# Kernel optimization log

Measured on AMD Instinct MI355X. Metric: run time of the kernel, lower is better.

The kernel has to match this reference:

```python
import jax, jax.numpy as jnp
import numpy as np

B, SEQ, P, D, H, DH, HID = 65536, 2, 1009, 256, 4, 64, 1024
ATT_RATE = 0.5

def setup_inputs() -> dict:
    key = jax.random.key(0)
    ks = jax.random.split(key, 18)
    init_range = 0.02
    lin = lambda k, shape, fan_in: jax.random.uniform(k, shape, jnp.float32, -1.0, 1.0) / np.sqrt(fan_in)
    return {
        "x": jax.random.randint(ks[0], (B, SEQ), 0, P),
        "tok_emb": jax.random.normal(ks[1], (P, D), jnp.float32) / np.sqrt(D),
        "pos_emb": jax.random.normal(ks[2], (SEQ, D), jnp.float32) / np.sqrt(D),
        "W_Q": init_range * jax.random.normal(ks[3], (H, D, DH), jnp.float32),
        "W_K": init_range * jax.random.normal(ks[4], (H, D, DH), jnp.float32),
        "W_V": init_range * jax.random.normal(ks[5], (H, D, DH), jnp.float32),
        "W_O": init_range * jax.random.normal(ks[6], (H, DH, D), jnp.float32),
        "b_Q": jnp.zeros((H, DH), jnp.float32),
        "b_K": jnp.zeros((H, DH), jnp.float32),
        "b_V": jnp.zeros((H, DH), jnp.float32),
        "b_O": jnp.zeros((D,), jnp.float32),
        "fc1_w": lin(ks[7], (HID, D), D),
        "fc1_b": lin(ks[8], (HID,), D),
        "fc2_w": lin(ks[9], (D, HID), HID),
        "fc2_b": lin(ks[10], (D,), HID),
        "un_w": lin(ks[11], (P, D), D),
        "un_b": lin(ks[12], (P,), D),
    }

def reference(x, tok_emb, pos_emb, W_Q, W_K, W_V, W_O, b_Q, b_K, b_V, b_O,
              fc1_w, fc1_b, fc2_w, fc2_b, un_w, un_b):
    # embed: [B, 2, D]
    h = tok_emb[x] + pos_emb[None, :, :]
    # attention (note: no residual, no layernorm in the original forward)
    q = jnp.einsum('bpd,hde->bphe', h, W_Q) + b_Q
    k = jnp.einsum('bpd,hde->bphe', h, W_K) + b_K
    v = jnp.einsum('bpd,hde->bphe', h, W_V) + b_V
    scores = jnp.einsum('bqhe,bkhe->bhqk', q, k) / np.sqrt(DH).astype(np.float32)
    pat = jax.nn.softmax(scores, axis=-1)
    pat = (1.0 - ATT_RATE) + ATT_RATE * pat  # blended softmax
    z = jnp.einsum('bkhe,bhqk->bqhe', v, pat)
    attn_out = jnp.einsum('bqhe,hed->bqd', z, W_O) + b_O
    # MLP (fc1/fc2, not the unused nn.Sequential)
    hid = jax.nn.relu(attn_out @ fc1_w.T + fc1_b)
    resid = hid @ fc2_w.T + fc2_b
    # unembed -> logits [B, 2, P]
    return resid @ un_w.T + un_b
```

## Files before the change

### kernel.cpp

```cpp
#include <hip/hip_runtime.h>

#define B_ 65536
#define SEQ_ 2
#define P_ 1009
#define D_ 256
#define H_ 4
#define DH_ 64
#define HID_ 1024

typedef unsigned short u16;
typedef __attribute__((ext_vector_type(8))) short short8;
typedef __attribute__((ext_vector_type(4))) float f32x4;

__device__ __forceinline__ u16 f2b(float f) {
  unsigned int u = __float_as_uint(f);
  u += 0x7fffu + ((u >> 16) & 1u);
  return (u16)(u >> 16);
}

__global__ __launch_bounds__(256) void prep_tables(
    const float* __restrict__ tok_emb, const float* __restrict__ pos_emb,
    const float* __restrict__ W_Q, const float* __restrict__ W_K,
    const float* __restrict__ W_V, const float* __restrict__ W_O,
    const float* __restrict__ b_Q, const float* __restrict__ b_K,
    const float* __restrict__ b_V,
    float* __restrict__ Qtab, float* __restrict__ Ktab,
    float* __restrict__ VOtab) {
  __shared__ float sh[D_];
  __shared__ float sv[D_];
  int blk = blockIdx.x;
  int t = blk >> 1, p = blk & 1;
  int j = threadIdx.x;
  sh[j] = tok_emb[t * D_ + j] + pos_emb[p * D_ + j];
  __syncthreads();
  int h = j >> 6, e = j & 63;
  float qv = b_Q[j], kv = b_K[j], vv = b_V[j];
  const float* wq = W_Q + h * (D_ * DH_) + e;
  const float* wk = W_K + h * (D_ * DH_) + e;
  const float* wvp = W_V + h * (D_ * DH_) + e;
  for (int k = 0; k < D_; ++k) {
    float hv = sh[k];
    qv += hv * wq[k * DH_];
    kv += hv * wk[k * DH_];
    vv += hv * wvp[k * DH_];
  }
  Qtab[blk * D_ + j] = qv;
  Ktab[blk * D_ + j] = kv;
  sv[j] = vv;
  __syncthreads();
  int d = j;
  for (int h2 = 0; h2 < H_; ++h2) {
    float acc = 0.f;
    const float* wo = W_O + h2 * (DH_ * D_) + d;
    for (int e2 = 0; e2 < DH_; ++e2) acc += sv[h2 * DH_ + e2] * wo[e2 * D_];
    VOtab[((size_t)blk * H_ + h2) * D_ + d] = acc;
  }
}

__global__ __launch_bounds__(256) void prep_weights(
    const float* __restrict__ fc1_w, const float* __restrict__ fc2_w,
    const float* __restrict__ un_w,
    u16* __restrict__ fc1b, u16* __restrict__ fc2b, u16* __restrict__ unb) {
  int i = blockIdx.x * 256 + threadIdx.x;
  fc1b[i] = f2b(fc1_w[i]);
  fc2b[i] = f2b(fc2_w[i]);
  int row = i >> 8;
  unb[i] = (row < P_) ? f2b(un_w[i]) : (u16)0;
}

__global__ __launch_bounds__(256) void attn_kernel(
    const int* __restrict__ x, const float* __restrict__ Qtab,
    const float* __restrict__ Ktab, const float* __restrict__ VOtab,
    const float* __restrict__ b_O, u16* __restrict__ attn_out) {
  __shared__ float sQ[2][D_];
  __shared__ float sK[2][D_];
  __shared__ float ssc[16];
  __shared__ float spat[16];
  int b = blockIdx.x;
  int t = threadIdx.x;
  int x0 = x[2 * b + 0];
  int x1 = x[2 * b + 1];
  sQ[0][t] = Qtab[(x0 * 2 + 0) * D_ + t];
  sQ[1][t] = Qtab[(x1 * 2 + 1) * D_ + t];
  sK[0][t] = Ktab[(x0 * 2 + 0) * D_ + t];
  sK[1][t] = Ktab[(x1 * 2 + 1) * D_ + t];
  __syncthreads();
  if (t < 16) {
    int h = t >> 2, i = (t >> 1) & 1, jj = t & 1;
    const float* q = &sQ[i][h * DH_];
    const float* k = &sK[jj][h * DH_];
    float s = 0.f;
    for (int e = 0; e < DH_; ++e) s += q[e] * k[e];
    ssc[t] = s * 0.125f;
  }
  __syncthreads();
  if (t < 8) {
    int h = t >> 1, i = t & 1;
    float s0 = ssc[h * 4 + i * 2 + 0];
    float s1 = ssc[h * 4 + i * 2 + 1];
    float m = fmaxf(s0, s1);
    float e0 = __expf(s0 - m), e1 = __expf(s1 - m);
    float inv = 1.f / (e0 + e1);
    spat[h * 4 + i * 2 + 0] = 0.5f + 0.5f * e0 * inv;
    spat[h * 4 + i * 2 + 1] = 0.5f + 0.5f * e1 * inv;
  }
  __syncthreads();
  int d = t;
  float bo = b_O[d];
  float o0 = bo, o1 = bo;
  for (int jj = 0; jj < 2; ++jj) {
    int xj = jj ? x1 : x0;
    const float* vo = VOtab + (size_t)(xj * 2 + jj) * (H_ * D_) + d;
    for (int h = 0; h < H_; ++h) {
      float v = vo[h * D_];
      o0 += spat[h * 4 + 0 + jj] * v;
      o1 += spat[h * 4 + 2 + jj] * v;
    }
  }
  attn_out[(size_t)(2 * b + 0) * D_ + d] = f2b(o0);
  attn_out[(size_t)(2 * b + 1) * D_ + d] = f2b(o1);
}

template <bool RELU, bool STORE_F32>
__global__ __launch_bounds__(256) void gemm_bt(
    const u16* __restrict__ A, const u16* __restrict__ Bt,
    const float* __restrict__ bias, void* __restrict__ Cout,
    int K, int ldc, int Neff) {
  __shared__ u16 lds_a[128 * 64];
  __shared__ u16 lds_b[128 * 64];
  int tid = threadIdx.x;
  int lane = tid & 63;
  int wv = tid >> 6;
  int wr = wv >> 1, wc = wv & 1;
  int m0 = blockIdx.x * 128;
  int n0 = blockIdx.y * 128;
  f32x4 acc[4][4] = {};
  int lr = lane >> 3;
  int lc = (lane & 7) * 8;
  int q = lane >> 4;
  int mrow = lane & 15;

  for (int k0 = 0; k0 < K; k0 += 64) {
#pragma unroll
    for (int i = 0; i < 4; ++i) {
      int row = i * 32 + wv * 8 + lr;
      const u16* g = A + (size_t)(m0 + row) * K + k0 + lc;
      __builtin_amdgcn_global_load_lds(
          (const __attribute__((address_space(1))) void*)g,
          (__attribute__((address_space(3))) void*)&lds_a[row * 64 + lc], 16, 0, 0);
    }
#pragma unroll
    for (int i = 0; i < 4; ++i) {
      int row = i * 32 + wv * 8 + lr;
      const u16* g = Bt + (size_t)(n0 + row) * K + k0 + lc;
      __builtin_amdgcn_global_load_lds(
          (const __attribute__((address_space(1))) void*)g,
          (__attribute__((address_space(3))) void*)&lds_b[row * 64 + lc], 16, 0, 0);
    }
    __syncthreads();
#pragma unroll
    for (int kk = 0; kk < 64; kk += 32) {
      short8 af[4], bfr[4];
#pragma unroll
      for (int tt = 0; tt < 4; ++tt)
        af[tt] = *(const short8*)&lds_a[(wr * 64 + tt * 16 + mrow) * 64 + kk + q * 8];
#pragma unroll
      for (int uu = 0; uu < 4; ++uu)
        bfr[uu] = *(const short8*)&lds_b[(wc * 64 + uu * 16 + mrow) * 64 + kk + q * 8];
#pragma unroll
      for (int tt = 0; tt < 4; ++tt)
#pragma unroll
        for (int uu = 0; uu < 4; ++uu)
          acc[tt][uu] = __builtin_amdgcn_mfma_f32_16x16x32_bf16(
              af[tt], bfr[uu], acc[tt][uu], 0, 0, 0);
    }
    __syncthreads();
  }

  int cn = lane & 15;
#pragma unroll
  for (int tt = 0; tt < 4; ++tt) {
    int gm = m0 + wr * 64 + tt * 16 + q * 4;
#pragma unroll
    for (int uu = 0; uu < 4; ++uu) {
      int gn = n0 + wc * 64 + uu * 16 + cn;
      if (gn < Neff) {
        float bv = bias[gn];
#pragma unroll
        for (int r = 0; r < 4; ++r) {
          float v = acc[tt][uu][r] + bv;
          if (RELU) v = fmaxf(v, 0.f);
          if (STORE_F32)
            ((float*)Cout)[(size_t)(gm + r) * ldc + gn] = v;
          else
            ((u16*)Cout)[(size_t)(gm + r) * ldc + gn] = f2b(v);
        }
      }
    }
  }
}

extern "C" void kernel_launch(void* const* d_in, const int* in_sizes, int n_in,
                              void* d_out, int out_size, void* d_ws, size_t ws_size,
                              hipStream_t stream) {
  const int* x = (const int*)d_in[0];
  const float* tok_emb = (const float*)d_in[1];
  const float* pos_emb = (const float*)d_in[2];
  const float* W_Q = (const float*)d_in[3];
  const float* W_K = (const float*)d_in[4];
  const float* W_V = (const float*)d_in[5];
  const float* W_O = (const float*)d_in[6];
  const float* b_Q = (const float*)d_in[7];
  const float* b_K = (const float*)d_in[8];
  const float* b_V = (const float*)d_in[9];
  const float* b_O = (const float*)d_in[10];
  const float* fc1_w = (const float*)d_in[11];
  const float* fc1_b = (const float*)d_in[12];
  const float* fc2_w = (const float*)d_in[13];
  const float* fc2_b = (const float*)d_in[14];
  const float* un_w = (const float*)d_in[15];
  const float* un_b = (const float*)d_in[16];

  char* ws = (char*)d_ws;
  size_t off = 0;
  auto alloc = [&](size_t bytes) {
    void* p = ws + off;
    off = (off + bytes + 255) & ~(size_t)255;
    return p;
  };
  float* Qtab = (float*)alloc((size_t)P_ * 2 * D_ * 4);
  float* Ktab = (float*)alloc((size_t)P_ * 2 * D_ * 4);
  float* VOtab = (float*)alloc((size_t)P_ * 2 * H_ * D_ * 4);
  u16* fc1b = (u16*)alloc((size_t)HID_ * D_ * 2);
  u16* fc2b = (u16*)alloc((size_t)D_ * HID_ * 2);
  u16* unb = (u16*)alloc((size_t)1024 * D_ * 2);
  u16* attn = (u16*)alloc((size_t)B_ * 2 * D_ * 2);
  u16* resid = (u16*)alloc((size_t)B_ * 2 * D_ * 2);
  u16* hid = (u16*)d_out;

  prep_tables<<<P_ * 2, 256, 0, stream>>>(tok_emb, pos_emb, W_Q, W_K, W_V, W_O,
                                          b_Q, b_K, b_V, Qtab, Ktab, VOtab);
  prep_weights<<<1024, 256, 0, stream>>>(fc1_w, fc2_w, un_w, fc1b, fc2b, unb);
  attn_kernel<<<B_, 256, 0, stream>>>(x, Qtab, Ktab, VOtab, b_O, attn);
  gemm_bt<true, false><<<dim3(1024, 8), 256, 0, stream>>>(attn, fc1b, fc1_b, hid, D_, HID_, HID_);
  gemm_bt<false, false><<<dim3(1024, 2), 256, 0, stream>>>(hid, fc2b, fc2_b, resid, HID_, D_, D_);
  gemm_bt<false, true><<<dim3(1024, 8), 256, 0, stream>>>(resid, unb, un_b, d_out, D_, P_, P_);
}
```

Baseline: 1.205 ms.

## Keep A tile in registers and stream swizzled B tiles through double-buffered LDS

```diff
diff --git a/kernel.cpp b/kernel.cpp
--- a/kernel.cpp
+++ b/kernel.cpp
@@ -62,10 +62,11 @@
     const float* __restrict__ un_w,
     u16* __restrict__ fc1b, u16* __restrict__ fc2b, u16* __restrict__ unb) {
   int i = blockIdx.x * 256 + threadIdx.x;
-  fc1b[i] = f2b(fc1_w[i]);
+  int n = i >> 8, k = i & 255;
+  int ksw = (((k >> 3) ^ (n & 7)) << 3) | (k & 7);
+  fc1b[n * 256 + ksw] = f2b(fc1_w[i]);
   fc2b[i] = f2b(fc2_w[i]);
-  int row = i >> 8;
-  unb[i] = (row < P_) ? f2b(un_w[i]) : (u16)0;
+  unb[n * 256 + ksw] = (n < P_) ? f2b(un_w[i]) : (u16)0;
 }
 
 __global__ __launch_bounds__(256) void attn_kernel(
@@ -197,6 +198,90 @@
         }
       }
     }
+  }
+}
+
+template <bool RELU, bool STORE_F32>
+__global__ __launch_bounds__(256, 2) void gemm_regA(
+    const u16* __restrict__ A, const u16* __restrict__ Bsw,
+    const float* __restrict__ bias, void* __restrict__ Cout,
+    int Ntiles, int ldc, int Neff) {
+  __shared__ u16 lb[2][64 * 256];
+  int tid = threadIdx.x;
+  int lane = tid & 63;
+  int wv = tid >> 6;
+  int wm = wv >> 1, wn = wv & 1;
+  int q = lane >> 4, mrow = lane & 15;
+  size_t m0 = (size_t)blockIdx.x * 128;
+
+  short8 af[4][8];
+#pragma unroll
+  for (int tt = 0; tt < 4; ++tt)
+#pragma unroll
+    for (int ks = 0; ks < 8; ++ks)
+      af[tt][ks] = *(const short8*)(A + (m0 + wm * 64 + tt * 16 + mrow) * 256 +
+                                    ks * 32 + q * 8);
+
+  auto stageB = [&](int bi, int nt) {
+#pragma unroll
+    for (int r2 = 0; r2 < 8; ++r2) {
+      int off = r2 * 2048 + tid * 8;
+      __builtin_amdgcn_global_load_lds(
+          (const __attribute__((address_space(1))) void*)(Bsw + (size_t)nt * (64 * 256) + off),
+          (__attribute__((address_space(3))) void*)(&lb[bi][off]), 16, 0, 0);
+    }
+  };
+
+  int rb0 = (wn * 32 + mrow) * 256;
+  int rb1 = rb0 + 16 * 256;
+  int s = mrow & 7;
+
+  auto tile = [&](int bi, int nt) {
+    const u16* bb = &lb[bi][0];
+    f32x4 acc[4][2] = {};
+#pragma unroll
+    for (int ks = 0; ks < 8; ++ks) {
+      int e = ((ks * 4 + q) ^ s) << 3;
+      short8 b0 = *(const short8*)(bb + rb0 + e);
+      short8 b1 = *(const short8*)(bb + rb1 + e);
+#pragma unroll
+      for (int tt = 0; tt < 4; ++tt) {
+        acc[tt][0] = __builtin_amdgcn_mfma_f32_16x16x32_bf16(af[tt][ks], b0, acc[tt][0], 0, 0, 0);
+        acc[tt][1] = __builtin_amdgcn_mfma_f32_16x16x32_bf16(af[tt][ks], b1, acc[tt][1], 0, 0, 0);
+      }
+    }
+    int n0 = nt * 64 + wn * 32;
+#pragma unroll
+    for (int uu = 0; uu < 2; ++uu) {
+      int gn = n0 + uu * 16 + mrow;
+      if (gn < Neff) {
+        float bv = bias[gn];
+#pragma unroll
+        for (int tt = 0; tt < 4; ++tt) {
+          size_t gm = m0 + wm * 64 + tt * 16 + q * 4;
+#pragma unroll
+          for (int r = 0; r < 4; ++r) {
+            float v = acc[tt][uu][r] + bv;
+            if (RELU) v = fmaxf(v, 0.f);
+            if (STORE_F32)
+              ((float*)Cout)[(gm + r) * ldc + gn] = v;
+            else
+              ((u16*)Cout)[(gm + r) * ldc + gn] = f2b(v);
+          }
+        }
+      }
+    }
+  };
+
+  stageB(0, 0);
+  __syncthreads();
+  for (int nt = 0; nt < Ntiles; nt += 2) {
+    if (nt + 1 < Ntiles) stageB(1, nt + 1);
+    tile(0, nt);
+    __syncthreads();
+    if (nt + 2 < Ntiles) stageB(0, nt + 2);
+    tile(1, nt + 1);
+    __syncthreads();
   }
 }
 
@@ -242,7 +327,7 @@
                                           b_Q, b_K, b_V, Qtab, Ktab, VOtab);
   prep_weights<<<1024, 256, 0, stream>>>(fc1_w, fc2_w, un_w, fc1b, fc2b, unb);
   attn_kernel<<<B_, 256, 0, stream>>>(x, Qtab, Ktab, VOtab, b_O, attn);
-  gemm_bt<true, false><<<dim3(1024, 8), 256, 0, stream>>>(attn, fc1b, fc1_b, hid, D_, HID_, HID_);
+  gemm_regA<true, false><<<1024, 256, 0, stream>>>(attn, fc1b, fc1_b, hid, 16, HID_, HID_);
   gemm_bt<false, false><<<dim3(1024, 2), 256, 0, stream>>>(hid, fc2b, fc2_b, resid, HID_, D_, D_);
-  gemm_bt<false, true><<<dim3(1024, 8), 256, 0, stream>>>(resid, unb, un_b, d_out, D_, P_, P_);
-}
+  gemm_regA<false, true><<<1024, 256, 0, stream>>>(resid, unb, un_b, d_out, 16, P_, P_);
+}
```

After: 1.117 ms. -7.3%, faster.
